# Kernel tuning notes

Measured on AMD Instinct MI355X. Metric: run time of the kernel, lower is better.

## Reference

```python
import jax, jax.numpy as jnp
import numpy as np

B, H, W, D, C, K, ITERS = 16, 64, 64, 64, 16, 5, 4
EPS_LN = 1e-5

def _ln(x, g, b):
    m = x.mean(-1, keepdims=True)
    v = jnp.mean((x - m) ** 2, axis=-1, keepdims=True)
    return (x - m) / jnp.sqrt(v + EPS_LN) * g + b

def _build_grid(h, w):
    # (h, w, 2) with x in [-1,1] over width, y in [-1,1] over height
    y, x = jnp.meshgrid(jnp.linspace(-1.0, 1.0, h), jnp.linspace(-1.0, 1.0, w), indexing='ij')
    return jnp.stack([x, y], axis=-1)

def _forward(feat, feat_color, mask, slot_noise, slots_mu, slots_logsigma,
             w_grid, b_grid, w_k, w_v, ln_kv_g, ln_kv_b, w_mlp, b_mlp,
             ln_q_g, ln_q_b, w_q, w_ih, w_hh, b_ih, b_hh,
             ln_feat_g, ln_feat_b, ln_color_g, ln_color_b,
             ln_res_g, ln_res_b, w_res, b_res):
    b, h, w, d = feat.shape
    n = h * w
    k_slots = mask.shape[0]
    scale = d ** (-0.5)

    grid = _build_grid(h, w)  # (H, W, 2)

    # fg position: weighted mean of grid under mask -> (K, 2), broadcast to (B, K, 2)
    gm = grid.transpose(2, 0, 1)[None] * mask            # (K, 2, H, W)
    fg_pos = gm.sum((2, 3)) / (mask.sum((2, 3)) + 1e-5)  # (K, 2)
    fg_pos = jnp.broadcast_to(fg_pos[None], (b, k_slots, 2))

    feat_n = _ln(feat.reshape(b, n, d), ln_feat_g, ln_feat_b)                    # (B, N, D)
    featc_n = _ln(feat_color.reshape(b, n, feat_color.shape[-1]), ln_color_g, ln_color_b)

    slot = slots_mu + jnp.exp(slots_logsigma) * slot_noise  # (B, K, D)

    # k/v with relative positional grid embedding (fg_pos is constant across iters,
    # so k/v are iteration-invariant and computed once -- same math as the original loop)
    rel = grid[None, None] - fg_pos[:, :, None, None, :]        # (B, K, H, W, 2)
    rel4 = jnp.concatenate([rel, -rel], -1).reshape(b, k_slots, n, 4)
    grid_embed = rel4 @ w_grid.T + b_grid                       # (B, K, N, D)
    k = _ln(feat_n @ w_k.T[None] [0][None][0][None][0] if False else (feat_n @ w_k.T)[:, None] + grid_embed, ln_kv_g, ln_kv_b) @ w_mlp.T + b_mlp
    v = _ln((feat_n @ w_v.T)[:, None] + grid_embed, ln_kv_g, ln_kv_b) @ w_mlp.T + b_mlp

    attn = None
    for it in range(ITERS):
        prev = slot
        q = _ln(slot, ln_q_g, ln_q_b) @ w_q.T                         # (B, K, D)
        logits = jnp.einsum('bkd,bknd->bkn', q, k) * scale
        attn = jax.nn.softmax(logits, axis=-1)                        # (B, K, N)
        upd = jnp.einsum('bkn,bknd->bkd', attn, v)                    # (B, K, D)
        if it != ITERS - 1:
            # torch GRUCell
            x = upd.reshape(-1, d)
            hp = slot.reshape(-1, d)
            gi = x @ w_ih.T + b_ih
            gh = hp @ w_hh.T + b_hh
            i_r, i_z, i_n = jnp.split(gi, 3, axis=-1)
            h_r, h_z, h_n = jnp.split(gh, 3, axis=-1)
            r = jax.nn.sigmoid(i_r + h_r)
            z = jax.nn.sigmoid(i_z + h_z)
            nn_ = jnp.tanh(i_n + r * h_n)
            slot = ((1.0 - z) * nn_ + z * hp).reshape(b, k_slots, d)
            slot = _ln(slot, ln_res_g, ln_res_b) @ w_res.T + b_res + prev
        else:
            slot_color = jnp.einsum('bkn,bnc->bkc', attn, featc_n)
            slot = jnp.concatenate([slot, slot_color], axis=-1)       # (B, K, D+C)

    amin = attn.min(axis=2, keepdims=True)
    amax = attn.max(axis=2, keepdims=True)
    attn = (attn - amin) / (amax - amin + 1e-5)
    return slot, fg_pos, attn

def setup_inputs() -> dict:
    key = jax.random.key(0)
    ks = jax.random.split(key, 16)
    def rn(i, shape, s=0.02):
        return jax.random.normal(ks[i], shape, jnp.float32) * s
    return {
        'feat': jax.random.normal(ks[0], (B, H, W, D), jnp.float32),
        'feat_color': jax.random.normal(ks[1], (B, H, W, C), jnp.float32),
        'mask': jax.random.uniform(ks[2], (K, 1, H, W), jnp.float32),
        'slot_noise': jax.random.normal(ks[3], (B, K, D), jnp.float32),
        'slots_mu': rn(4, (1, 1, D), 1.0),
        'slots_logsigma': rn(5, (1, 1, D), 0.01),
        'w_grid': rn(6, (D, 4)), 'b_grid': jnp.zeros((D,), jnp.float32),
        'w_k': rn(7, (D, D)), 'w_v': rn(8, (D, D)),
        'ln_kv_g': jnp.ones((D,), jnp.float32), 'ln_kv_b': jnp.zeros((D,), jnp.float32),
        'w_mlp': rn(9, (D, D)), 'b_mlp': jnp.zeros((D,), jnp.float32),
        'ln_q_g': jnp.ones((D,), jnp.float32), 'ln_q_b': jnp.zeros((D,), jnp.float32),
        'w_q': rn(10, (D, D)),
        'w_ih': rn(11, (3 * D, D)), 'w_hh': rn(12, (3 * D, D)),
        'b_ih': jnp.zeros((3 * D,), jnp.float32), 'b_hh': jnp.zeros((3 * D,), jnp.float32),
        'ln_feat_g': jnp.ones((D,), jnp.float32), 'ln_feat_b': jnp.zeros((D,), jnp.float32),
        'ln_color_g': jnp.ones((C,), jnp.float32), 'ln_color_b': jnp.zeros((C,), jnp.float32),
        'ln_res_g': jnp.ones((D,), jnp.float32), 'ln_res_b': jnp.zeros((D,), jnp.float32),
        'w_res': rn(13, (D, D)), 'b_res': jnp.zeros((D,), jnp.float32),
    }

def reference(feat, feat_color, mask, slot_noise, slots_mu, slots_logsigma,
              w_grid, b_grid, w_k, w_v, ln_kv_g, ln_kv_b, w_mlp, b_mlp,
              ln_q_g, ln_q_b, w_q, w_ih, w_hh, b_ih, b_hh,
              ln_feat_g, ln_feat_b, ln_color_g, ln_color_b,
              ln_res_g, ln_res_b, w_res, b_res):
    return _forward(feat, feat_color, mask, slot_noise, slots_mu, slots_logsigma,
                    w_grid, b_grid, w_k, w_v, ln_kv_g, ln_kv_b, w_mlp, b_mlp,
                    ln_q_g, ln_q_b, w_q, w_ih, w_hh, b_ih, b_hh,
                    ln_feat_g, ln_feat_b, ln_color_g, ln_color_b,
                    ln_res_g, ln_res_b, w_res, b_res)
```

## Files before the change

### kernel.cpp

```cpp
#include <hip/hip_runtime.h>
#include <stdint.h>

#define B_ 16
#define H_ 64
#define W_ 64
#define D_ 64
#define C_ 16
#define K_ 5
#define N_ 4096
#define NC_ 8
#define CS_ 512
#define EPS 1e-5f

typedef __attribute__((ext_vector_type(8))) short bf16x8;
typedef __attribute__((ext_vector_type(4))) float f32x4;

__device__ __forceinline__ float wsum64(float v){
  #pragma unroll
  for(int o=1;o<64;o<<=1) v += __shfl_xor(v,o,64);
  return v;
}
__device__ __forceinline__ float wmax64(float v){
  #pragma unroll
  for(int o=1;o<64;o<<=1) v = fmaxf(v, __shfl_xor(v,o,64));
  return v;
}
__device__ __forceinline__ float wmin64(float v){
  #pragma unroll
  for(int o=1;o<64;o<<=1) v = fminf(v, __shfl_xor(v,o,64));
  return v;
}
__device__ __forceinline__ uint16_t f2bf(float f){
  uint32_t u = __float_as_uint(f);
  u += 0x7fffu + ((u>>16)&1u);
  return (uint16_t)(u>>16);
}

__global__ __launch_bounds__(256) void k_pre(
    const float* __restrict__ mask, const float* __restrict__ noise,
    const float* __restrict__ mu, const float* __restrict__ lsg,
    const float* __restrict__ wm, const float* __restrict__ bm, const float* __restrict__ lnkb,
    const float* __restrict__ wk, const float* __restrict__ wv, const float* __restrict__ lnfb,
    const float* __restrict__ wq, const float* __restrict__ lnqg, const float* __restrict__ lnqb,
    const float* __restrict__ wres, const float* __restrict__ bres,
    const float* __restrict__ lnrg, const float* __restrict__ lnrb,
    const float* __restrict__ wih, const float* __restrict__ whh,
    const float* __restrict__ wg, const float* __restrict__ bg,
    float* __restrict__ ws_fg, float* __restrict__ out_fg,
    float* __restrict__ bm2, float* __restrict__ fkb, float* __restrict__ fvb,
    float* __restrict__ qb, float* __restrict__ br2,
    float* __restrict__ wgx, float* __restrict__ wgy, float* __restrict__ gscal,
    float* __restrict__ wqpT, float* __restrict__ wrpT,
    float* __restrict__ wvT, float* __restrict__ wmT,
    float* __restrict__ gw, float* __restrict__ slot){
  int bid=blockIdx.x, tid=threadIdx.x;
  if(bid<5){
    int k=bid;
    float sm=0.f, sx=0.f, sy=0.f;
    for(int p=tid; p<H_*W_; p+=256){
      int i=p>>6, j=p&63;
      float m = mask[k*H_*W_ + p];
      float x = -1.f + (2.f/63.f)*j;
      float y = -1.f + (2.f/63.f)*i;
      sm+=m; sx+=m*x; sy+=m*y;
    }
    __shared__ float r0[4], r1[4], r2[4];
    int wid=tid>>6, lane=tid&63;
    sm=wsum64(sm); sx=wsum64(sx); sy=wsum64(sy);
    if(lane==0){ r0[wid]=sm; r1[wid]=sx; r2[wid]=sy; }
    __syncthreads();
    if(tid==0){
      float tm=r0[0]+r0[1]+r0[2]+r0[3];
      float tx=r1[0]+r1[1]+r1[2]+r1[3];
      float ty=r2[0]+r2[1]+r2[2]+r2[3];
      float px = tx/(tm+1e-5f), py = ty/(tm+1e-5f);
      ws_fg[k*2+0]=px; ws_fg[k*2+1]=py;
      for(int b=0;b<B_;b++){ out_fg[(b*K_+k)*2+0]=px; out_fg[(b*K_+k)*2+1]=py; }
    }
  } else if(bid==5){
    int sel=tid>>6, o=tid&63; float s=0.f;
    if(sel==0){ s=bm[o]; for(int d=0;d<64;d++) s+=lnkb[d]*wm[o*64+d]; bm2[o]=s; }
    else if(sel==1){ for(int d=0;d<64;d++) s+=lnqb[d]*wq[o*64+d]; qb[o]=0.125f*s; }
    else if(sel==2){ for(int d=0;d<64;d++) s+=lnrb[d]*wres[o*64+d]; br2[o]=s+bres[o]; }
    else { for(int d=0;d<64;d++) s+=lnfb[d]*wk[o*64+d]; fkb[o]=s; }
  } else if(bid==6){
    int wv4=tid>>6, l=tid&63;
    if(wv4==0){ float s=0.f; for(int d=0;d<64;d++) s+=lnfb[d]*wv[l*64+d]; fvb[l]=s; }
    else if(wv4==1){
      float4 w4 = *(const float4*)(wg + l*4);
      wgx[l]=w4.x-w4.z; wgy[l]=w4.y-w4.w;
    } else if(wv4==2){
      float4 w4 = *(const float4*)(wg + l*4);
      float wx=w4.x-w4.z, wy=w4.y-w4.w, bl=bg[l];
      float t;
      t=wsum64(wx);    if(l==0) gscal[0]=t*(1.f/64.f);
      t=wsum64(wy);    if(l==0) gscal[1]=t*(1.f/64.f);
      t=wsum64(bl);    if(l==0) gscal[2]=t*(1.f/64.f);
      t=wsum64(wx*wx); if(l==0) gscal[3]=t*(1.f/64.f);
      t=wsum64(wy*wy); if(l==0) gscal[4]=t*(1.f/64.f);
      t=wsum64(wx*wy); if(l==0) gscal[5]=t*(2.f/64.f);
      t=wsum64(wx*bl); if(l==0) gscal[6]=t*(2.f/64.f);
      t=wsum64(wy*bl); if(l==0) gscal[7]=t*(2.f/64.f);
      t=wsum64(bl*bl); if(l==0) gscal[8]=t*(1.f/64.f);
    }
  } else if(bid<71){
    int i=(bid-7)*256+tid;
    int a=i>>12, r=i&4095, d=r>>6, o=r&63;
    if(a==0)      wqpT[r]=0.125f*lnqg[d]*wq[o*64+d];
    else if(a==1) wrpT[r]=lnrg[d]*wres[o*64+d];
    else if(a==2) wvT[r]=wv[o*64+d];
    else          wmT[r]=wm[o*64+d];
  } else if(bid<167){
    int i=(bid-71)*256+tid;
    int g6=i>>12, r=i&4095, d=r>>6, o=r&63;
    float v = (g6<3)? wih[(g6*64+o)*64+d] : whh[((g6-3)*64+o)*64+d];
    gw[g6*4096 + d*64 + o] = v;
  } else {
    int i=(bid-167)*256+tid;
    if(i<B_*K_*D_){ int d=i&63; slot[i]=mu[d]+expf(lsg[d])*noise[i]; }
  }
}

__global__ __launch_bounds__(256) void k_featln(const float* __restrict__ feat,
    const float* __restrict__ wk, const float* __restrict__ wv, const float* __restrict__ gf,
    const float* __restrict__ fkb, const float* __restrict__ fvb,
    const float* __restrict__ wgx, const float* __restrict__ wgy, const float* __restrict__ bg,
    const float* __restrict__ fc, const float* __restrict__ gc, const float* __restrict__ bc,
    uint16_t* __restrict__ Aout, float4* __restrict__ kstat, float4* __restrict__ vstat,
    float* __restrict__ fcn){
  int tid=threadIdx.x, wid=tid>>6, lane=tid&63;
  int q=lane>>4, c=lane&15;
  size_t row = (size_t)blockIdx.x*64 + wid*16 + c;
  const float* xp = feat + row*64;
  float x[16];
  *(float4*)&x[0]  = *(const float4*)(xp + q*8);
  *(float4*)&x[4]  = *(const float4*)(xp + q*8 + 4);
  *(float4*)&x[8]  = *(const float4*)(xp + 32 + q*8);
  *(float4*)&x[12] = *(const float4*)(xp + 36 + q*8);
  float s=0.f;
  #pragma unroll
  for(int i=0;i<16;i++) s+=x[i];
  s += __shfl_xor(s,16,64); s += __shfl_xor(s,32,64);
  float mean = s*(1.f/64.f);
  float v=0.f;
  #pragma unroll
  for(int i=0;i<16;i++){ float d=x[i]-mean; v+=d*d; }
  v += __shfl_xor(v,16,64); v += __shfl_xor(v,32,64);
  float rs = rsqrtf(v*(1.f/64.f)+EPS);
  float gl[16];
  *(float4*)&gl[0]  = *(const float4*)(gf + q*8);
  *(float4*)&gl[4]  = *(const float4*)(gf + q*8 + 4);
  *(float4*)&gl[8]  = *(const float4*)(gf + 32 + q*8);
  *(float4*)&gl[12] = *(const float4*)(gf + 36 + q*8);
  bf16x8 A0, A1;
  #pragma unroll
  for(int j=0;j<8;j++){
    A0[j] = (short)f2bf((x[j]  -mean)*rs);
    A1[j] = (short)f2bf((x[8+j]-mean)*rs);
  }
  *(bf16x8*)(Aout + row*64 + q*8) = A0;
  *(bf16x8*)(Aout + row*64 + 32 + q*8) = A1;
  float wgxl[4][4], wgyl[4][4], bgl[4][4];
  #pragma unroll
  for(int ot=0;ot<4;ot++){
    *(float4*)&wgxl[ot][0] = *(const float4*)(wgx + ot*16 + q*4);
    *(float4*)&wgyl[ot][0] = *(const float4*)(wgy + ot*16 + q*4);
    *(float4*)&bgl[ot][0]  = *(const float4*)(bg + ot*16 + q*4);
  }
  #pragma unroll
  for(int mat=0;mat<2;mat++){
    const float* w = mat? wv : wk;
    const float* fb = mat? fvb : fkb;
    float ss=0.f, s2=0.f, dx=0.f, dy=0.f, db=0.f;
    #pragma unroll
    for(int ot=0; ot<4; ot++){
      const float* wp = w + (size_t)(ot*16+c)*64 + q*8;
      bf16x8 W0, W1;
      #pragma unroll
      for(int j=0;j<8;j++){ W0[j]=(short)f2bf(wp[j]*gl[j]); W1[j]=(short)f2bf(wp[32+j]*gl[8+j]); }
      float4 bq = *(const float4*)(fb + ot*16 + q*4);
      f32x4 acc = {bq.x,bq.y,bq.z,bq.w};
      acc = __builtin_amdgcn_mfma_f32_16x16x32_bf16(W0, A0, acc, 0,0,0);
      acc = __builtin_amdgcn_mfma_f32_16x16x32_bf16(W1, A1, acc, 0,0,0);
      #pragma unroll
      for(int r=0;r<4;r++){
        float a=acc[r];
        ss+=a; s2+=a*a;
        dx = fmaf(a, wgxl[ot][r], dx);
        dy = fmaf(a, wgyl[ot][r], dy);
        db = fmaf(a, bgl[ot][r], db);
      }
    }
    ss += __shfl_xor(ss,16,64); ss += __shfl_xor(ss,32,64);
    s2 += __shfl_xor(s2,16,64); s2 += __shfl_xor(s2,32,64);
    dx += __shfl_xor(dx,16,64); dx += __shfl_xor(dx,32,64);
    dy += __shfl_xor(dy,16,64); dy += __shfl_xor(dy,32,64);
    db += __shfl_xor(db,16,64); db += __shfl_xor(db,32,64);
    if(lane<16){
      size_t row2 = (size_t)blockIdx.x*64 + wid*16 + lane;
      float4 st = { ss*(1.f/64.f), s2*(1.f/64.f)+db*(1.f/32.f), dx*(1.f/32.f), dy*(1.f/32.f) };
      (mat? vstat : kstat)[row2] = st;
    }
  }
  int r16=tid>>4, cc=tid&15;
  #pragma unroll
  for(int i=0;i<4;i++){
    size_t row2 = (size_t)blockIdx.x*64 + i*16 + r16;
    float xv = fc[row2*16+cc];
    float sc=xv;
    #pragma unroll
    for(int o=1;o<16;o<<=1) sc += __shfl_xor(sc,o,16);
    float m2 = sc*(1.f/16.f);
    float df = xv-m2;
    float v2 = df*df;
    #pragma unroll
    for(int o=1;o<16;o<<=1) v2 += __shfl_xor(v2,o,16);
    fcn[row2*16+cc] = df*rsqrtf(v2*(1.f/16.f)+EPS)*gc[cc] + bc[cc];
  }
}

template<bool GRU, bool FINAL>
__global__ __launch_bounds__(256) void k_attn(const uint16_t* __restrict__ Aw,
    const float4* __restrict__ kstat, const float4* __restrict__ vstat,
    const float* __restrict__ slot_prev, float* __restrict__ slot_cur,
    const float* __restrict__ part, const float* __restrict__ pscal,
    const float* __restrict__ red_in,
    const float* __restrict__ gw,
    const float* __restrict__ bih, const float* __restrict__ bhh,
    const float* __restrict__ wrpT, const float* __restrict__ br2,
    const float* __restrict__ wqpT, const float* __restrict__ qb,
    const float* __restrict__ wm, const float* __restrict__ wk,
    const float* __restrict__ lnfg, const float* __restrict__ lnkg,
    const float* __restrict__ fkb, const float* __restrict__ bm2, const float* __restrict__ fvb,
    const float* __restrict__ wvT, const float* __restrict__ wmT,
    const float* __restrict__ wgx, const float* __restrict__ wgy, const float* __restrict__ bg,
    const float* __restrict__ gscal, const float* __restrict__ ws_fg,
    float* __restrict__ lgt, float* __restrict__ red_out,
    float* __restrict__ part_o, float* __restrict__ pscal_o){
  __shared__ float vv[64], vh[64], qs[64];
  __shared__ float cst[8];
  __shared__ float red6[4][64][6];
  __shared__ float rm[4], rn[4];
  __shared__ float rsc[4][5];
  __shared__ float ps[CS_];
  __shared__ float pw[4][64];
  int chunk=blockIdx.x, bk=blockIdx.y, b=bk/K_, k=bk-b*K_;
  int tid=threadIdx.x, wid=tid>>6, lane=tid&63, sub=lane>>4, c4=lane&15;
  int o=lane, qq=wid;
  float mwgx=gscal[0], mwgy=gscal[1], mbg=gscal[2];
  float g1=gscal[3], g2=gscal[4], g3=gscal[5], g4=gscal[6], g5=gscal[7], g6=gscal[8];
  float fgx=ws_fg[k*2+0], fgy=ws_fg[k*2+1];

  #define MV(Wptr) { float p_=0.f; \
      _Pragma("unroll") \
      for(int dd=0;dd<16;dd++) p_ = fmaf(vv[qq*16+dd], (Wptr)[(qq*16+dd)*64+o], p_); \
      red6[qq][o][0]=p_; } __syncthreads();
  #define SUM0 (red6[0][lane][0]+red6[1][lane][0]+red6[2][lane][0]+red6[3][lane][0])

  float cur=0.f, qv=0.f, qp=0.f, hp=0.f;
  if(GRU){
    float As=0.f, Ax=0.f, Ay=0.f, Am=0.f;
    if(wid==0){
      float mred[NC_], sred[NC_];
      #pragma unroll
      for(int cc=0;cc<NC_;cc++){
        const float* rp = red_in + ((size_t)bk*NC_+cc)*4;
        mred[cc]=rp[0]; sred[cc]=rp[1];
      }
      float M=-1e30f;
      #pragma unroll
      for(int cc=0;cc<NC_;cc++) M=fmaxf(M,mred[cc]);
      float S=0.f;
      #pragma unroll
      for(int cc=0;cc<NC_;cc++){ mred[cc]=__expf(mred[cc]-M); S=fmaf(sred[cc],mred[cc],S); }
      float invS=1.f/S;
      float sA=0.f;
      #pragma unroll
      for(int cc=0;cc<NC_;cc++){
        float lam = mred[cc]*invS;
        sA = fmaf(lam, part[((size_t)bk*NC_+cc)*64+lane], sA);
        const float* pp = pscal + ((size_t)bk*NC_+cc)*4;
        As=fmaf(lam,pp[0],As); Ax=fmaf(lam,pp[1],Ax);
        Ay=fmaf(lam,pp[2],Ay); Am=fmaf(lam,pp[3],Am);
      }
      vv[lane] = lnfg[lane]*sA;
    }
    __syncthreads();
    MV(wvT);
    if(wid==0){
      float fvs = SUM0 + fvb[lane]*As;
      float zs = fvs + Ax*wgx[lane] + Ay*wgy[lane] + As*bg[lane] - Am;
      vv[lane] = lnkg[lane]*zs;
    }
    __syncthreads();
    MV(wmT);
    if(wid==0){
      float x_ = SUM0 + bm2[lane];
      hp = slot_prev[bk*64+lane];
      vv[lane]=x_; vh[lane]=hp;
    }
    __syncthreads();
    {
      float p0=0.f,p1=0.f,p2=0.f,p3=0.f,p4=0.f,p5=0.f;
      #pragma unroll
      for(int dd=0;dd<16;dd++){
        int d = qq*16+dd;
        float xd=vv[d], hd=vh[d];
        p0 = fmaf(xd, gw[d*64+o], p0);
        p1 = fmaf(xd, gw[4096+d*64+o], p1);
        p2 = fmaf(xd, gw[8192+d*64+o], p2);
        p3 = fmaf(hd, gw[12288+d*64+o], p3);
        p4 = fmaf(hd, gw[16384+d*64+o], p4);
        p5 = fmaf(hd, gw[20480+d*64+o], p5);
      }
      red6[qq][o][0]=p0; red6[qq][o][1]=p1; red6[qq][o][2]=p2;
      red6[qq][o][3]=p3; red6[qq][o][4]=p4; red6[qq][o][5]=p5;
    }
    __syncthreads();
    if(wid==0){
      float gir=bih[lane],      giz=bih[64+lane],   gin=bih[128+lane];
      float ghr=bhh[lane],      ghz=bhh[64+lane],   ghn=bhh[128+lane];
      #pragma unroll
      for(int w=0;w<4;w++){
        gir+=red6[w][lane][0]; giz+=red6[w][lane][1]; gin+=red6[w][lane][2];
        ghr+=red6[w][lane][3]; ghz+=red6[w][lane][4]; ghn+=red6[w][lane][5];
      }
      float r=1.f/(1.f+__expf(-(gir+ghr)));
      float z=1.f/(1.f+__expf(-(giz+ghz)));
      float nn=tanhf(gin+r*ghn);
      float sp=(1.f-z)*nn+z*hp;
      float m=wsum64(sp)*(1.f/64.f); float df=sp-m;
      float var=wsum64(df*df)*(1.f/64.f);
      vv[lane]=df*rsqrtf(var+EPS);
    }
    __syncthreads();
    MV(wrpT);
    if(wid==0){
      cur = SUM0 + br2[lane] + hp;
      if(chunk==0) slot_cur[bk*64+lane]=cur;
    }
  } else {
    if(wid==0) cur = slot_prev[bk*64+lane];
  }
  __syncthreads();
  if(wid==0){
    float m=wsum64(cur)*(1.f/64.f); float df=cur-m;
    float var=wsum64(df*df)*(1.f/64.f);
    vv[lane]=df*rsqrtf(var+EPS);
  }
  __syncthreads();
  MV(wqpT);
  if(wid==0){ qv = SUM0 + qb[lane]; vv[lane]=qv; }
  __syncthreads();
  MV(wm);
  if(wid==0){ qp = SUM0*lnkg[lane]; vv[lane]=qp; }
  __syncthreads();
  MV(wk);
  if(wid==0){
    qs[lane] = SUM0*lnfg[lane];
    float s1 = wsum64(qp);
    float c1 = wsum64(qp*wgx[lane]);
    float c2 = wsum64(qp*wgy[lane]);
    float c3 = wsum64(qp*(bg[lane]+fkb[lane]));
    float c4c = wsum64(qv*bm2[lane]);
    if(lane==0){
      cst[0]=c1-s1*mwgx; cst[1]=c2-s1*mwgy; cst[2]=c3-s1*mbg; cst[3]=s1; cst[4]=c4c;
    }
  }
  __syncthreads();
  #undef MV
  #undef SUM0

  float CX=cst[0], CY=cst[1], C0=cst[2], S1=cst[3], C4=cst[4];

  const uint2* Ab2 = (const uint2*)Aw + (size_t)b*N_*16 + (size_t)chunk*CS_*16;
  float q0=qs[c4*4+0], q1=qs[c4*4+1], q2=qs[c4*4+2], q3=qs[c4*4+3];
  for(int t=0;t<32;t++){
    int n = wid*128 + t*4 + sub;
    uint2 u = Ab2[(size_t)n*16 + c4];
    float d0 = __uint_as_float(u.x<<16)*q0 + __uint_as_float(u.x&0xffff0000u)*q1
             + __uint_as_float(u.y<<16)*q2 + __uint_as_float(u.y&0xffff0000u)*q3;
    d0 += __shfl_xor(d0,1,64); d0 += __shfl_xor(d0,2,64);
    d0 += __shfl_xor(d0,4,64); d0 += __shfl_xor(d0,8,64);
    if(c4==0) ps[n] = d0;
  }
  __syncthreads();

  const float4* ks = kstat + (size_t)b*N_ + chunk*CS_;
  const float4* vs = vstat + (size_t)b*N_ + chunk*CS_;
  float l[2], rsv[2], rxv[2], ryv[2], muv[2];
  #pragma unroll
  for(int i=0;i<2;i++){
    int nl = tid + i*256;
    int n = chunk*CS_ + nl;
    float dot = ps[nl];
    float rx = (-1.f + (2.f/63.f)*(n&63)) - fgx;
    float ry = (-1.f + (2.f/63.f)*(n>>6)) - fgy;
    float4 st = ks[nl];
    float mu = st.x + rx*mwgx + ry*mwgy + mbg;
    float var = st.y + rx*st.z + ry*st.w
              + (g1*rx*rx + g2*ry*ry + g3*rx*ry + g4*rx + g5*ry + g6) - mu*mu;
    float rsn = rsqrtf(var + EPS);
    float a = rsn*(dot + rx*CX + ry*CY + C0 - S1*st.x) + C4;
    l[i]=a;
    if(FINAL) lgt[(size_t)bk*N_ + n] = a;
    if(!FINAL){
      float4 sv = vs[nl];
      float muV = sv.x + rx*mwgx + ry*mwgy + mbg;
      float varV = sv.y + rx*sv.z + ry*sv.w
                 + (g1*rx*rx + g2*ry*ry + g3*rx*ry + g4*rx + g5*ry + g6) - muV*muV;
      rsv[i] = rsqrtf(varV + EPS);
      rxv[i]=rx; ryv[i]=ry; muv[i]=muV;
    }
  }
  float wm_ = wmax64(fmaxf(l[0],l[1]));
  if(lane==0) rm[wid]=wm_;
  if(FINAL){ float mn=wmin64(fminf(l[0],l[1])); if(lane==0) rn[wid]=mn; }
  __syncthreads();
  float m_c = fmaxf(fmaxf(rm[0],rm[1]),fmaxf(rm[2],rm[3]));
  float e0=__expf(l[0]-m_c), e1=__expf(l[1]-m_c);
  float sc=e0+e1;
  float As2=0.f, Ax2=0.f, Ay2=0.f, Am2=0.f;
  if(!FINAL){
    float w0=e0*rsv[0], w1=e1*rsv[1];
    ps[tid]=w0; ps[tid+256]=w1;
    As2=w0+w1;
    Ax2=fmaf(w0,rxv[0],w1*rxv[1]);
    Ay2=fmaf(w0,ryv[0],w1*ryv[1]);
    Am2=fmaf(w0,muv[0],w1*muv[1]);
  }
  sc=wsum64(sc);
  if(!FINAL){ As2=wsum64(As2); Ax2=wsum64(Ax2); Ay2=wsum64(Ay2); Am2=wsum64(Am2); }
  if(lane==0){ rsc[wid][0]=sc; rsc[wid][1]=As2; rsc[wid][2]=Ax2; rsc[wid][3]=Ay2; rsc[wid][4]=Am2; }
  __syncthreads();
  if(tid==0){
    float* rp = red_out + ((size_t)bk*NC_+chunk)*4;
    rp[0]=m_c;
    rp[1]=rsc[0][0]+rsc[1][0]+rsc[2][0]+rsc[3][0];
    if(FINAL) rp[2]=fminf(fminf(rn[0],rn[1]),fminf(rn[2],rn[3]));
    if(!FINAL){
      float* pp = pscal_o + ((size_t)bk*NC_+chunk)*4;
      pp[0]=rsc[0][1]+rsc[1][1]+rsc[2][1]+rsc[3][1];
      pp[1]=rsc[0][2]+rsc[1][2]+rsc[2][2]+rsc[3][2];
      pp[2]=rsc[0][3]+rsc[1][3]+rsc[2][3]+rsc[3][3];
      pp[3]=rsc[0][4]+rsc[1][4]+rsc[2][4]+rsc[3][4];
    }
  }
  if(!FINAL){
    float a0=0.f,a1=0.f,a2=0.f,a3=0.f;
    for(int t=0;t<32;t++){
      int n = wid*128 + t*4 + sub;
      float w = ps[n];
      uint2 u = Ab2[(size_t)n*16 + c4];
      a0 += w*__uint_as_float(u.x<<16);
      a1 += w*__uint_as_float(u.x&0xffff0000u);
      a2 += w*__uint_as_float(u.y<<16);
      a3 += w*__uint_as_float(u.y&0xffff0000u);
    }
    a0+=__shfl_xor(a0,16,64); a0+=__shfl_xor(a0,32,64);
    a1+=__shfl_xor(a1,16,64); a1+=__shfl_xor(a1,32,64);
    a2+=__shfl_xor(a2,16,64); a2+=__shfl_xor(a2,32,64);
    a3+=__shfl_xor(a3,16,64); a3+=__shfl_xor(a3,32,64);
    if(lane<16){
      pw[wid][lane*4+0]=a0; pw[wid][lane*4+1]=a1;
      pw[wid][lane*4+2]=a2; pw[wid][lane*4+3]=a3;
    }
    __syncthreads();
    if(tid<64){
      part_o[((size_t)bk*NC_+chunk)*64 + tid] = pw[0][tid]+pw[1][tid]+pw[2][tid]+pw[3][tid];
    }
  }
}

__global__ __launch_bounds__(256) void k_fin(const float* __restrict__ lgt,
    const float* __restrict__ red, const float* __restrict__ featc,
    float* __restrict__ partc, float* __restrict__ out_attn){
  __shared__ float psp[CS_];
  __shared__ float pcz[4][16];
  int chunk=blockIdx.x, bk=blockIdx.y, b=bk/K_;
  int tid=threadIdx.x, wid=tid>>6, lane=tid&63, sub=lane>>4, c4=lane&15;
  const float* rp = red + (size_t)bk*NC_*4;
  float M=-1e30f;
  #pragma unroll
  for(int i=0;i<NC_;i++) M = fmaxf(M, rp[i*4]);
  float S=0.f;
  #pragma unroll
  for(int i=0;i<NC_;i++) S += rp[i*4+1]*__expf(rp[i*4]-M);
  float invS = 1.f/S;
  float LMIN=1e30f;
  #pragma unroll
  for(int i=0;i<NC_;i++) LMIN=fminf(LMIN, rp[i*4+2]);
  float amin = __expf(LMIN-M)*invS;
  float dinv = 1.f/(invS - amin + 1e-5f);
  const float* lp = lgt + (size_t)bk*N_ + chunk*CS_;
  #pragma unroll
  for(int i=0;i<2;i++){
    int nl = tid + i*256;
    float p = __expf(lp[nl]-M)*invS;
    psp[nl]=p;
    out_attn[(size_t)bk*N_ + chunk*CS_ + nl] = (p - amin)*dinv;
  }
  __syncthreads();
  const float* Fb = featc + ((size_t)b*N_ + chunk*CS_)*16;
  float ac=0.f;
  for(int t=0;t<32;t++){
    int n = wid*128 + t*4 + sub;
    ac += psp[n]*Fb[(size_t)n*16 + c4];
  }
  ac+=__shfl_xor(ac,16,64); ac+=__shfl_xor(ac,32,64);
  if(lane<16) pcz[wid][lane]=ac;
  __syncthreads();
  if(tid<16){
    partc[((size_t)bk*NC_+chunk)*16 + tid] = pcz[0][tid]+pcz[1][tid]+pcz[2][tid]+pcz[3][tid];
  }
}

__global__ __launch_bounds__(64) void k_final(const float* __restrict__ slot,
    const float* __restrict__ partc, float* __restrict__ out_slot){
  int bk=blockIdx.x, lane=threadIdx.x;
  out_slot[bk*80+lane]=slot[bk*64+lane];
  if(lane<16){
    float s=0.f;
    #pragma unroll
    for(int cch=0;cch<NC_;cch++) s += partc[((size_t)bk*NC_+cch)*16+lane];
    out_slot[bk*80+64+lane]=s;
  }
}

extern "C" void kernel_launch(void* const* d_in, const int* in_sizes, int n_in,
                              void* d_out, int out_size, void* d_ws, size_t ws_size,
                              hipStream_t stream){
  (void)in_sizes; (void)n_in; (void)out_size; (void)ws_size;
  const float* feat = (const float*)d_in[0];
  const float* featc= (const float*)d_in[1];
  const float* mask = (const float*)d_in[2];
  const float* noise= (const float*)d_in[3];
  const float* mu   = (const float*)d_in[4];
  const float* lsg  = (const float*)d_in[5];
  const float* wg   = (const float*)d_in[6];
  const float* bg   = (const float*)d_in[7];
  const float* wk   = (const float*)d_in[8];
  const float* wv   = (const float*)d_in[9];
  const float* lnkg = (const float*)d_in[10];
  const float* lnkb = (const float*)d_in[11];
  const float* wm   = (const float*)d_in[12];
  const float* bm   = (const float*)d_in[13];
  const float* lnqg = (const float*)d_in[14];
  const float* lnqb = (const float*)d_in[15];
  const float* wq   = (const float*)d_in[16];
  const float* wih  = (const float*)d_in[17];
  const float* whh  = (const float*)d_in[18];
  const float* bih  = (const float*)d_in[19];
  const float* bhh  = (const float*)d_in[20];
  const float* lnfg = (const float*)d_in[21];
  const float* lnfb = (const float*)d_in[22];
  const float* lncg = (const float*)d_in[23];
  const float* lncb = (const float*)d_in[24];
  const float* lnrg = (const float*)d_in[25];
  const float* lnrb = (const float*)d_in[26];
  const float* wres = (const float*)d_in[27];
  const float* bres = (const float*)d_in[28];

  float* out = (float*)d_out;
  float* out_slot = out;
  float* out_fg   = out + 6400;
  float* out_attn = out + 6560;

  float* wsf     = (float*)d_ws;
  float* ws_fg   = wsf;
  float* ws_bm2  = wsf + 16;
  float* ws_fkb  = ws_bm2 + 64;
  float* ws_fvb  = ws_fkb + 64;
  float* ws_qb   = ws_fvb + 64;
  float* ws_br2  = ws_qb + 64;
  float* ws_wgx  = ws_br2 + 64;
  float* ws_wgy  = ws_wgx + 64;
  float* ws_gs   = ws_wgy + 64;
  float* ws_wqpT = ws_gs + 16;
  float* ws_wrpT = ws_wqpT + 4096;
  float* ws_wvT  = ws_wrpT + 4096;
  float* ws_wmT  = ws_wvT + 4096;
  float* ws_gw   = ws_wmT + 4096;
  float* ws_fc   = ws_gw + 24576;
  float* ws_sl0  = ws_fc + (size_t)B_*N_*C_;
  float* ws_sl1  = ws_sl0 + B_*K_*D_;
  float* ws_lgt  = ws_sl1 + B_*K_*D_;
  float* ws_red0 = ws_lgt + (size_t)B_*K_*N_;
  float* ws_red1 = ws_red0 + B_*K_*NC_*4;
  float* ws_prt0 = ws_red1 + B_*K_*NC_*4;
  float* ws_prt1 = ws_prt0 + (size_t)B_*K_*NC_*64;
  float* ws_psc0 = ws_prt1 + (size_t)B_*K_*NC_*64;
  float* ws_psc1 = ws_psc0 + B_*K_*NC_*4;
  float* ws_pc   = ws_psc1 + B_*K_*NC_*4;
  float4* ws_kst = (float4*)(ws_pc + B_*K_*NC_*16);
  float4* ws_vst = ws_kst + (size_t)B_*N_;
  uint16_t* ws_A = (uint16_t*)(ws_vst + (size_t)B_*N_);

  k_pre<<<187,256,0,stream>>>(mask,noise,mu,lsg, wm,bm,lnkb, wk,wv,lnfb,
                              wq,lnqg,lnqb, wres,bres,lnrg,lnrb, wih,whh, wg,bg,
                              ws_fg,out_fg, ws_bm2,ws_fkb,ws_fvb,ws_qb,ws_br2,
                              ws_wgx,ws_wgy,ws_gs,
                              ws_wqpT,ws_wrpT,ws_wvT,ws_wmT, ws_gw, ws_sl0);
  k_featln<<<(B_*N_)/64,256,0,stream>>>(feat,wk,wv,lnfg,ws_fkb,ws_fvb,
                                        ws_wgx,ws_wgy,bg,
                                        featc,lncg,lncb,
                                        ws_A,ws_kst,ws_vst,ws_fc);

  dim3 agrid(NC_,B_*K_);
  #define ATTN_ARGS(SPREV,SCUR,PIN,SCIN,RIN,ROUT,POUT,SCOUT) \
      ws_A,ws_kst,ws_vst,SPREV,SCUR,PIN,SCIN,RIN,ws_gw, \
      bih,bhh,ws_wrpT,ws_br2,ws_wqpT,ws_qb, wm,wk,lnfg,lnkg, \
      ws_fkb,ws_bm2,ws_fvb, ws_wvT,ws_wmT, ws_wgx,ws_wgy,bg, ws_gs,ws_fg, \
      ws_lgt,ROUT,POUT,SCOUT

  k_attn<false,false><<<agrid,256,0,stream>>>(ATTN_ARGS(ws_sl0,ws_sl0,ws_prt1,ws_psc1,ws_red1,ws_red0,ws_prt0,ws_psc0));
  k_attn<true,false><<<agrid,256,0,stream>>>(ATTN_ARGS(ws_sl0,ws_sl1,ws_prt0,ws_psc0,ws_red0,ws_red1,ws_prt1,ws_psc1));
  k_attn<true,false><<<agrid,256,0,stream>>>(ATTN_ARGS(ws_sl1,ws_sl0,ws_prt1,ws_psc1,ws_red1,ws_red0,ws_prt0,ws_psc0));
  k_attn<true,true><<<agrid,256,0,stream>>>(ATTN_ARGS(ws_sl0,ws_sl1,ws_prt0,ws_psc0,ws_red0,ws_red1,ws_prt1,ws_psc1));
  k_fin<<<agrid,256,0,stream>>>(ws_lgt,ws_red1,ws_fc,ws_pc,out_attn);
  k_final<<<B_*K_,64,0,stream>>>(ws_sl1, ws_pc, out_slot);
}
```

Baseline: 239.8 us.

## Split slot update from attention and share feature tile across all slots with MFMA

Moves the per-slot GRU/query computation into its own small kernel launched once per (batch, slot), instead of recomputing it redundantly in every chunk block. The attention kernel is now gridded over (chunk, batch) and stages the bf16 feature tile in shared memory once for all 5 slots. It computes the q·A dot products with bf16 MFMA and reuses the staged tile for the weighted aggregation. Chunk count is doubled to keep enough blocks busy. The cost is four extra kernel launches, a global round-trip for q and constants, and bf16 rounding of q in the MFMA path.

```diff
diff --git a/kernel.cpp b/kernel.cpp
--- a/kernel.cpp
+++ b/kernel.cpp
@@ -8,8 +8,8 @@
 #define C_ 16
 #define K_ 5
 #define N_ 4096
-#define NC_ 8
-#define CS_ 512
+#define NC_ 16
+#define CS_ 256
 #define EPS 1e-5f
 
 typedef __attribute__((ext_vector_type(8))) short bf16x8;
@@ -219,9 +219,8 @@
   }
 }
 
-template<bool GRU, bool FINAL>
-__global__ __launch_bounds__(256) void k_attn(const uint16_t* __restrict__ Aw,
-    const float4* __restrict__ kstat, const float4* __restrict__ vstat,
+template<bool GRU>
+__global__ __launch_bounds__(256) void k_slotq(
     const float* __restrict__ slot_prev, float* __restrict__ slot_cur,
     const float* __restrict__ part, const float* __restrict__ pscal,
     const float* __restrict__ red_in,
@@ -234,22 +233,14 @@
     const float* __restrict__ fkb, const float* __restrict__ bm2, const float* __restrict__ fvb,
     const float* __restrict__ wvT, const float* __restrict__ wmT,
     const float* __restrict__ wgx, const float* __restrict__ wgy, const float* __restrict__ bg,
-    const float* __restrict__ gscal, const float* __restrict__ ws_fg,
-    float* __restrict__ lgt, float* __restrict__ red_out,
-    float* __restrict__ part_o, float* __restrict__ pscal_o){
-  __shared__ float vv[64], vh[64], qs[64];
-  __shared__ float cst[8];
+    const float* __restrict__ gscal,
+    float* __restrict__ qs_out, float* __restrict__ cst_out){
+  __shared__ float vv[64], vh[64];
   __shared__ float red6[4][64][6];
-  __shared__ float rm[4], rn[4];
-  __shared__ float rsc[4][5];
-  __shared__ float ps[CS_];
-  __shared__ float pw[4][64];
-  int chunk=blockIdx.x, bk=blockIdx.y, b=bk/K_, k=bk-b*K_;
-  int tid=threadIdx.x, wid=tid>>6, lane=tid&63, sub=lane>>4, c4=lane&15;
+  int bk=blockIdx.x;
+  int tid=threadIdx.x, wid=tid>>6, lane=tid&63;
   int o=lane, qq=wid;
   float mwgx=gscal[0], mwgy=gscal[1], mbg=gscal[2];
-  float g1=gscal[3], g2=gscal[4], g3=gscal[5], g4=gscal[6], g5=gscal[7], g6=gscal[8];
-  float fgx=ws_fg[k*2+0], fgy=ws_fg[k*2+1];
 
   #define MV(Wptr) { float p_=0.f; \
       _Pragma("unroll") \
@@ -318,8 +309,8 @@
     }
     __syncthreads();
     if(wid==0){
-      float gir=bih[lane],      giz=bih[64+lane],   gin=bih[128+lane];
-      float ghr=bhh[lane],      ghz=bhh[64+lane],   ghn=bhh[128+lane];
+      float gir=bih[lane], giz=bih[64+lane], gin=bih[128+lane];
+      float ghr=bhh[lane], ghz=bhh[64+lane], ghn=bhh[128+lane];
       #pragma unroll
       for(int w=0;w<4;w++){
         gir+=red6[w][lane][0]; giz+=red6[w][lane][1]; gin+=red6[w][lane][2];
@@ -337,7 +328,7 @@
     MV(wrpT);
     if(wid==0){
       cur = SUM0 + br2[lane] + hp;
-      if(chunk==0) slot_cur[bk*64+lane]=cur;
+      slot_cur[bk*64+lane]=cur;
     }
   } else {
     if(wid==0) cur = slot_prev[bk*64+lane];
@@ -357,117 +348,151 @@
   __syncthreads();
   MV(wk);
   if(wid==0){
-    qs[lane] = SUM0*lnfg[lane];
+    qs_out[bk*64+lane] = SUM0*lnfg[lane];
     float s1 = wsum64(qp);
     float c1 = wsum64(qp*wgx[lane]);
     float c2 = wsum64(qp*wgy[lane]);
     float c3 = wsum64(qp*(bg[lane]+fkb[lane]));
     float c4c = wsum64(qv*bm2[lane]);
     if(lane==0){
-      cst[0]=c1-s1*mwgx; cst[1]=c2-s1*mwgy; cst[2]=c3-s1*mbg; cst[3]=s1; cst[4]=c4c;
-    }
-  }
-  __syncthreads();
+      float* cp = cst_out + bk*8;
+      cp[0]=c1-s1*mwgx; cp[1]=c2-s1*mwgy; cp[2]=c3-s1*mbg; cp[3]=s1; cp[4]=c4c;
+    }
+  }
   #undef MV
   #undef SUM0
-
-  float CX=cst[0], CY=cst[1], C0=cst[2], S1=cst[3], C4=cst[4];
-
-  const uint2* Ab2 = (const uint2*)Aw + (size_t)b*N_*16 + (size_t)chunk*CS_*16;
-  float q0=qs[c4*4+0], q1=qs[c4*4+1], q2=qs[c4*4+2], q3=qs[c4*4+3];
-  for(int t=0;t<32;t++){
-    int n = wid*128 + t*4 + sub;
-    uint2 u = Ab2[(size_t)n*16 + c4];
-    float d0 = __uint_as_float(u.x<<16)*q0 + __uint_as_float(u.x&0xffff0000u)*q1
-             + __uint_as_float(u.y<<16)*q2 + __uint_as_float(u.y&0xffff0000u)*q3;
-    d0 += __shfl_xor(d0,1,64); d0 += __shfl_xor(d0,2,64);
-    d0 += __shfl_xor(d0,4,64); d0 += __shfl_xor(d0,8,64);
-    if(c4==0) ps[n] = d0;
-  }
-  __syncthreads();
-
-  const float4* ks = kstat + (size_t)b*N_ + chunk*CS_;
-  const float4* vs = vstat + (size_t)b*N_ + chunk*CS_;
-  float l[2], rsv[2], rxv[2], ryv[2], muv[2];
-  #pragma unroll
-  for(int i=0;i<2;i++){
-    int nl = tid + i*256;
-    int n = chunk*CS_ + nl;
-    float dot = ps[nl];
-    float rx = (-1.f + (2.f/63.f)*(n&63)) - fgx;
-    float ry = (-1.f + (2.f/63.f)*(n>>6)) - fgy;
-    float4 st = ks[nl];
+}
+
+template<bool FINAL>
+__global__ __launch_bounds__(256) void k_attn(const uint16_t* __restrict__ Aw,
+    const float4* __restrict__ kstat, const float4* __restrict__ vstat,
+    const float* __restrict__ qsg, const float* __restrict__ cstg,
+    const float* __restrict__ gscal, const float* __restrict__ ws_fg,
+    float* __restrict__ lgt, float* __restrict__ red_out,
+    float* __restrict__ part_o, float* __restrict__ pscal_o){
+  __shared__ uint32_t As_[CS_*32];
+  __shared__ float dps[5][CS_+1];
+  __shared__ float pw[4][5][64];
+  __shared__ float rm[4], rn[4];
+  __shared__ float rsc[4][5];
+  __shared__ float cstl[5][5];
+  __shared__ float fgl[5][2];
+  int chunk=blockIdx.x, b=blockIdx.y;
+  int tid=threadIdx.x, wid=tid>>6, lane=tid&63;
+  int c=lane&15, q=lane>>4;
+  float mwgx=gscal[0], mwgy=gscal[1], mbg=gscal[2];
+  float g1=gscal[3], g2=gscal[4], g3=gscal[5], g4=gscal[6], g5=gscal[7], g6=gscal[8];
+
+  const uint4* Ag = (const uint4*)(Aw + ((size_t)b*N_ + chunk*CS_)*64);
+  #pragma unroll
+  for(int jj=0;jj<8;jj++){
+    int f = jj*256 + tid;
+    uint4 u = Ag[f];
+    *(uint4*)(As_ + f*4) = u;
+  }
+  if(tid<25) cstl[tid/5][tid%5] = cstg[(b*K_ + tid/5)*8 + (tid%5)];
+  if(tid>=32 && tid<42){ int i2=tid-32; fgl[i2>>1][i2&1] = ws_fg[i2]; }
+  __syncthreads();
+
+  {
+    bf16x8 QF0={0,0,0,0,0,0,0,0}, QF1={0,0,0,0,0,0,0,0};
+    if(c<5){
+      const float* qpp = qsg + (b*K_+c)*64;
+      #pragma unroll
+      for(int j=0;j<8;j++){
+        QF0[j] = (short)f2bf(qpp[q*8+j]);
+        QF1[j] = (short)f2bf(qpp[32+q*8+j]);
+      }
+    }
+    const uint16_t* Abase = Aw + ((size_t)b*N_ + chunk*CS_)*64;
+    #pragma unroll
+    for(int it=0;it<4;it++){
+      int tile = wid*64 + it*16;
+      const uint16_t* rp = Abase + (size_t)(tile+c)*64;
+      bf16x8 BF0 = *(const bf16x8*)(rp + q*8);
+      bf16x8 BF1 = *(const bf16x8*)(rp + 32 + q*8);
+      f32x4 acc = {0.f,0.f,0.f,0.f};
+      acc = __builtin_amdgcn_mfma_f32_16x16x32_bf16(QF0, BF0, acc, 0,0,0);
+      acc = __builtin_amdgcn_mfma_f32_16x16x32_bf16(QF1, BF1, acc, 0,0,0);
+      #pragma unroll
+      for(int r=0;r<4;r++){
+        int s = q*4+r;
+        if(s<5) dps[s][tile+c]=acc[r];
+      }
+    }
+  }
+  __syncthreads();
+
+  int t = tid;
+  int n = chunk*CS_ + t;
+  float4 st = kstat[(size_t)b*N_ + n];
+  float4 sv;
+  if(!FINAL) sv = vstat[(size_t)b*N_ + n];
+  float gx = -1.f + (2.f/63.f)*(n&63);
+  float gy = -1.f + (2.f/63.f)*(n>>6);
+  #pragma unroll
+  for(int k=0;k<5;k++){
+    float rx = gx - fgl[k][0], ry = gy - fgl[k][1];
+    float CX=cstl[k][0], CY=cstl[k][1], C0=cstl[k][2], S1=cstl[k][3], C4=cstl[k][4];
+    float quad = g1*rx*rx + g2*ry*ry + g3*rx*ry + g4*rx + g5*ry + g6;
     float mu = st.x + rx*mwgx + ry*mwgy + mbg;
-    float var = st.y + rx*st.z + ry*st.w
-              + (g1*rx*rx + g2*ry*ry + g3*rx*ry + g4*rx + g5*ry + g6) - mu*mu;
-    float rsn = rsqrtf(var + EPS);
-    float a = rsn*(dot + rx*CX + ry*CY + C0 - S1*st.x) + C4;
-    l[i]=a;
-    if(FINAL) lgt[(size_t)bk*N_ + n] = a;
+    float var = st.y + rx*st.z + ry*st.w + quad - mu*mu;
+    float rsn = rsqrtf(var+EPS);
+    float l = rsn*(dps[k][t] + rx*CX + ry*CY + C0 - S1*st.x) + C4;
+    float wmx = wmax64(l);
+    if(lane==0) rm[wid]=wmx;
+    if(FINAL){ float mn=wmin64(l); if(lane==0) rn[wid]=mn; }
+    __syncthreads();
+    float m_c = fmaxf(fmaxf(rm[0],rm[1]),fmaxf(rm[2],rm[3]));
+    float e = __expf(l-m_c);
+    float scq=e, As2=0.f, Ax2=0.f, Ay2=0.f, Am2=0.f, w_=0.f;
     if(!FINAL){
-      float4 sv = vs[nl];
       float muV = sv.x + rx*mwgx + ry*mwgy + mbg;
-      float varV = sv.y + rx*sv.z + ry*sv.w
-                 + (g1*rx*rx + g2*ry*ry + g3*rx*ry + g4*rx + g5*ry + g6) - muV*muV;
-      rsv[i] = rsqrtf(varV + EPS);
-      rxv[i]=rx; ryv[i]=ry; muv[i]=muV;
-    }
-  }
-  float wm_ = wmax64(fmaxf(l[0],l[1]));
-  if(lane==0) rm[wid]=wm_;
-  if(FINAL){ float mn=wmin64(fminf(l[0],l[1])); if(lane==0) rn[wid]=mn; }
-  __syncthreads();
-  float m_c = fmaxf(fmaxf(rm[0],rm[1]),fmaxf(rm[2],rm[3]));
-  float e0=__expf(l[0]-m_c), e1=__expf(l[1]-m_c);
-  float sc=e0+e1;
-  float As2=0.f, Ax2=0.f, Ay2=0.f, Am2=0.f;
+      float varV = sv.y + rx*sv.z + ry*sv.w + quad - muV*muV;
+      float rsv_ = rsqrtf(varV+EPS);
+      w_ = e*rsv_;
+      As2=w_; Ax2=w_*rx; Ay2=w_*ry; Am2=w_*muV;
+    } else {
+      lgt[(size_t)(b*K_+k)*N_ + n] = l;
+    }
+    scq=wsum64(scq);
+    if(!FINAL){ As2=wsum64(As2); Ax2=wsum64(Ax2); Ay2=wsum64(Ay2); Am2=wsum64(Am2); }
+    if(lane==0){ rsc[wid][0]=scq; rsc[wid][1]=As2; rsc[wid][2]=Ax2; rsc[wid][3]=Ay2; rsc[wid][4]=Am2; }
+    __syncthreads();
+    if(tid==0){
+      size_t idx = ((size_t)(b*K_+k)*NC_+chunk)*4;
+      red_out[idx+0]=m_c;
+      red_out[idx+1]=rsc[0][0]+rsc[1][0]+rsc[2][0]+rsc[3][0];
+      if(FINAL) red_out[idx+2]=fminf(fminf(rn[0],rn[1]),fminf(rn[2],rn[3]));
+      if(!FINAL){
+        pscal_o[idx+0]=rsc[0][1]+rsc[1][1]+rsc[2][1]+rsc[3][1];
+        pscal_o[idx+1]=rsc[0][2]+rsc[1][2]+rsc[2][2]+rsc[3][2];
+        pscal_o[idx+2]=rsc[0][3]+rsc[1][3]+rsc[2][3]+rsc[3][3];
+        pscal_o[idx+3]=rsc[0][4]+rsc[1][4]+rsc[2][4]+rsc[3][4];
+      }
+    }
+    if(!FINAL) dps[k][t]=w_;
+  }
+
   if(!FINAL){
-    float w0=e0*rsv[0], w1=e1*rsv[1];
-    ps[tid]=w0; ps[tid+256]=w1;
-    As2=w0+w1;
-    Ax2=fmaf(w0,rxv[0],w1*rxv[1]);
-    Ay2=fmaf(w0,ryv[0],w1*ryv[1]);
-    Am2=fmaf(w0,muv[0],w1*muv[1]);
-  }
-  sc=wsum64(sc);
-  if(!FINAL){ As2=wsum64(As2); Ax2=wsum64(Ax2); Ay2=wsum64(Ay2); Am2=wsum64(Am2); }
-  if(lane==0){ rsc[wid][0]=sc; rsc[wid][1]=As2; rsc[wid][2]=Ax2; rsc[wid][3]=Ay2; rsc[wid][4]=Am2; }
-  __syncthreads();
-  if(tid==0){
-    float* rp = red_out + ((size_t)bk*NC_+chunk)*4;
-    rp[0]=m_c;
-    rp[1]=rsc[0][0]+rsc[1][0]+rsc[2][0]+rsc[3][0];
-    if(FINAL) rp[2]=fminf(fminf(rn[0],rn[1]),fminf(rn[2],rn[3]));
-    if(!FINAL){
-      float* pp = pscal_o + ((size_t)bk*NC_+chunk)*4;
-      pp[0]=rsc[0][1]+rsc[1][1]+rsc[2][1]+rsc[3][1];
-      pp[1]=rsc[0][2]+rsc[1][2]+rsc[2][2]+rsc[3][2];
-      pp[2]=rsc[0][3]+rsc[1][3]+rsc[2][3]+rsc[3][3];
-      pp[3]=rsc[0][4]+rsc[1][4]+rsc[2][4]+rsc[3][4];
-    }
-  }
-  if(!FINAL){
-    float a0=0.f,a1=0.f,a2=0.f,a3=0.f;
-    for(int t=0;t<32;t++){
-      int n = wid*128 + t*4 + sub;
-      float w = ps[n];
-      uint2 u = Ab2[(size_t)n*16 + c4];
-      a0 += w*__uint_as_float(u.x<<16);
-      a1 += w*__uint_as_float(u.x&0xffff0000u);
-      a2 += w*__uint_as_float(u.y<<16);
-      a3 += w*__uint_as_float(u.y&0xffff0000u);
-    }
-    a0+=__shfl_xor(a0,16,64); a0+=__shfl_xor(a0,32,64);
-    a1+=__shfl_xor(a1,16,64); a1+=__shfl_xor(a1,32,64);
-    a2+=__shfl_xor(a2,16,64); a2+=__shfl_xor(a2,32,64);
-    a3+=__shfl_xor(a3,16,64); a3+=__shfl_xor(a3,32,64);
-    if(lane<16){
-      pw[wid][lane*4+0]=a0; pw[wid][lane*4+1]=a1;
-      pw[wid][lane*4+2]=a2; pw[wid][lane*4+3]=a3;
-    }
+    __syncthreads();
+    const uint16_t* Au = (const uint16_t*)As_;
+    float a[5]={0.f,0.f,0.f,0.f,0.f};
+    for(int r64=0;r64<64;r64++){
+      int row = wid*64 + r64;
+      float av = __uint_as_float(((uint32_t)Au[row*64+lane])<<16);
+      #pragma unroll
+      for(int k=0;k<5;k++) a[k]=fmaf(dps[k][row], av, a[k]);
+    }
+    #pragma unroll
+    for(int k=0;k<5;k++) pw[wid][k][lane]=a[k];
     __syncthreads();
     if(tid<64){
-      part_o[((size_t)bk*NC_+chunk)*64 + tid] = pw[0][tid]+pw[1][tid]+pw[2][tid]+pw[3][tid];
+      #pragma unroll
+      for(int k=0;k<5;k++){
+        float s2 = pw[0][k][tid]+pw[1][k][tid]+pw[2][k][tid]+pw[3][k][tid];
+        part_o[((size_t)(b*K_+k)*NC_+chunk)*64 + tid] = s2;
+      }
     }
   }
 }
@@ -493,18 +518,16 @@
   float amin = __expf(LMIN-M)*invS;
   float dinv = 1.f/(invS - amin + 1e-5f);
   const float* lp = lgt + (size_t)bk*N_ + chunk*CS_;
-  #pragma unroll
-  for(int i=0;i<2;i++){
-    int nl = tid + i*256;
-    float p = __expf(lp[nl]-M)*invS;
-    psp[nl]=p;
-    out_attn[(size_t)bk*N_ + chunk*CS_ + nl] = (p - amin)*dinv;
+  {
+    float p = __expf(lp[tid]-M)*invS;
+    psp[tid]=p;
+    out_attn[(size_t)bk*N_ + chunk*CS_ + tid] = (p - amin)*dinv;
   }
   __syncthreads();
   const float* Fb = featc + ((size_t)b*N_ + chunk*CS_)*16;
   float ac=0.f;
-  for(int t=0;t<32;t++){
-    int n = wid*128 + t*4 + sub;
+  for(int t=0;t<16;t++){
+    int n = wid*64 + t*4 + sub;
     ac += psp[n]*Fb[(size_t)n*16 + c4];
   }
   ac+=__shfl_xor(ac,16,64); ac+=__shfl_xor(ac,32,64);
@@ -584,7 +607,9 @@
   float* ws_fc   = ws_gw + 24576;
   float* ws_sl0  = ws_fc + (size_t)B_*N_*C_;
   float* ws_sl1  = ws_sl0 + B_*K_*D_;
-  float* ws_lgt  = ws_sl1 + B_*K_*D_;
+  float* ws_qs   = ws_sl1 + B_*K_*D_;
+  float* ws_cst  = ws_qs + B_*K_*D_;
+  float* ws_lgt  = ws_cst + 640;
   float* ws_red0 = ws_lgt + (size_t)B_*K_*N_;
   float* ws_red1 = ws_red0 + B_*K_*NC_*4;
   float* ws_prt0 = ws_red1 + B_*K_*NC_*4;
@@ -606,17 +631,21 @@
                                         featc,lncg,lncb,
                                         ws_A,ws_kst,ws_vst,ws_fc);
 
-  dim3 agrid(NC_,B_*K_);
-  #define ATTN_ARGS(SPREV,SCUR,PIN,SCIN,RIN,ROUT,POUT,SCOUT) \
-      ws_A,ws_kst,ws_vst,SPREV,SCUR,PIN,SCIN,RIN,ws_gw, \
+  dim3 agrid(NC_,B_);
+  #define SQ_ARGS(SPREV,SCUR,PIN,SCIN,RIN) SPREV,SCUR,PIN,SCIN,RIN,ws_gw, \
       bih,bhh,ws_wrpT,ws_br2,ws_wqpT,ws_qb, wm,wk,lnfg,lnkg, \
-      ws_fkb,ws_bm2,ws_fvb, ws_wvT,ws_wmT, ws_wgx,ws_wgy,bg, ws_gs,ws_fg, \
+      ws_fkb,ws_bm2,ws_fvb, ws_wvT,ws_wmT, ws_wgx,ws_wgy,bg, ws_gs, ws_qs,ws_cst
+  #define AT_ARGS(ROUT,POUT,SCOUT) ws_A,ws_kst,ws_vst,ws_qs,ws_cst,ws_gs,ws_fg, \
       ws_lgt,ROUT,POUT,SCOUT
 
-  k_attn<false,false><<<agrid,256,0,stream>>>(ATTN_ARGS(ws_sl0,ws_sl0,ws_prt1,ws_psc1,ws_red1,ws_red0,ws_prt0,ws_psc0));
-  k_attn<true,false><<<agrid,256,0,stream>>>(ATTN_ARGS(ws_sl0,ws_sl1,ws_prt0,ws_psc0,ws_red0,ws_red1,ws_prt1,ws_psc1));
-  k_attn<true,false><<<agrid,256,0,stream>>>(ATTN_ARGS(ws_sl1,ws_sl0,ws_prt1,ws_psc1,ws_red1,ws_red0,ws_prt0,ws_psc0));
-  k_attn<true,true><<<agrid,256,0,stream>>>(ATTN_ARGS(ws_sl0,ws_sl1,ws_prt0,ws_psc0,ws_red0,ws_red1,ws_prt1,ws_psc1));
-  k_fin<<<agrid,256,0,stream>>>(ws_lgt,ws_red1,ws_fc,ws_pc,out_attn);
+  k_slotq<false><<<B_*K_,256,0,stream>>>(SQ_ARGS(ws_sl0,ws_sl0,ws_prt1,ws_psc1,ws_red1));
+  k_attn<false><<<agrid,256,0,stream>>>(AT_ARGS(ws_red0,ws_prt0,ws_psc0));
+  k_slotq<true><<<B_*K_,256,0,stream>>>(SQ_ARGS(ws_sl0,ws_sl1,ws_prt0,ws_psc0,ws_red0));
+  k_attn<false><<<agrid,256,0,stream>>>(AT_ARGS(ws_red1,ws_prt1,ws_psc1));
+  k_slotq<true><<<B_*K_,256,0,stream>>>(SQ_ARGS(ws_sl1,ws_sl0,ws_prt1,ws_psc1,ws_red1));
+  k_attn<false><<<agrid,256,0,stream>>>(AT_ARGS(ws_red0,ws_prt0,ws_psc0));
+  k_slotq<true><<<B_*K_,256,0,stream>>>(SQ_ARGS(ws_sl0,ws_sl1,ws_prt0,ws_psc0,ws_red0));
+  k_attn<true><<<agrid,256,0,stream>>>(AT_ARGS(ws_red1,ws_prt1,ws_psc1));
+  k_fin<<<dim3(NC_,B_*K_),256,0,stream>>>(ws_lgt,ws_red1,ws_fc,ws_pc,out_attn);
   k_final<<<B_*K_,64,0,stream>>>(ws_sl1, ws_pc, out_slot);
 }
```

Result: faster. 224.0 us (-6.6%).
